# Performance work log

Measured on AMD Instinct MI355X. Metric: run time of the kernel, lower is better.

## Reference

```python
import math
import jax, jax.numpy as jnp
import numpy as np

B, S, D, H = 128, 512, 768, 12
DH = D // H  # 64


def setup_inputs() -> dict:
    key = jax.random.key(0)
    k1, k2, k3, k4, k5 = jax.random.split(key, 5)
    return {
        "X": jax.random.normal(k1, (B, S, D), jnp.float32),
        "W_qkv": jax.random.normal(k2, (3 * D, D), jnp.float32) * 0.02,
        "b_qkv": jax.random.normal(k3, (3 * D,), jnp.float32) * 0.02,
        "W_dense": jax.random.normal(k4, (D, D), jnp.float32) * 0.02,
        "b_dense": jax.random.normal(k5, (D,), jnp.float32) * 0.02,
    }


def reference(X, W_qkv, b_qkv, W_dense, b_dense):
    # Faithful translation of SelfAttention.forward (including its unusual
    # seq/batch layout: scores are [S*H, B, B] and the tril mask FILLS the
    # lower triangle with -10000, exactly as masked_fill_(tril, -1e4) does).
    b, s, d = X.shape
    qkv = jnp.einsum('bsd,ed->bse', X, W_qkv) + b_qkv            # [B,S,3D]
    qkv = qkv.reshape(b, s, H, 3 * DH)
    q = qkv[..., :DH]
    k = qkv[..., DH:2 * DH]
    v = qkv[..., 2 * DH:]
    q = q.reshape(b, s * H, DH).transpose(1, 0, 2)               # [S*H,B,DH]
    k = k.reshape(b, s * H, DH).transpose(1, 0, 2)
    v = v.reshape(b, s * H, DH).transpose(1, 0, 2)
    scores = jnp.einsum('nbd,ncd->nbc', q, k) / math.sqrt(DH)    # [S*H,B,B]
    scores = scores.reshape(s, H, b, b)
    tril = jnp.tril(jnp.ones((s, b, b), bool))[:, None]          # [S,1,B,B]
    scores = jnp.where(tril, jnp.float32(-10000.0), scores)
    probs = jax.nn.softmax(scores, axis=-1).reshape(s * H, b, b)
    ctx = jnp.einsum('nbc,ncd->nbd', probs, v)                   # [S*H,B,DH]
    ctx = ctx.reshape(s, H, b, DH).transpose(2, 0, 1, 3).reshape(b, s, d)
    out = jnp.einsum('bsd,ed->bse', ctx, W_dense)                # bias NOT added
    return (out, b_dense)
```

## Files before the change

kernel.cpp:

```cpp
#include <hip/hip_runtime.h>
#include <hip/hip_bf16.h>
#include <cstdint>
#include <cstddef>


typedef __attribute__((ext_vector_type(8))) short bf16x8_t;
typedef __attribute__((ext_vector_type(4))) float f32x4_t;

__device__ inline unsigned short f2bf(float x) {
  union { float f; unsigned int u; } v; v.f = x;
  return (unsigned short)((v.u + 0x7FFFu + ((v.u >> 16) & 1u)) >> 16);
}

#define GLL16(gp, lp) __builtin_amdgcn_global_load_lds(                      \
    (const __attribute__((address_space(1))) void*)(gp),                     \
    (__attribute__((address_space(3))) void*)(lp), 16, 0, 0)

__device__ __forceinline__ void bar() {
  asm volatile("" ::: "memory");
  __builtin_amdgcn_s_barrier();
  asm volatile("" ::: "memory");
}
#define WAITV(n) asm volatile("s_waitcnt vmcnt(" #n ")" ::: "memory")

__global__ __launch_bounds__(256) void cvt_kernel(const float* __restrict__ in,
                                                  unsigned short* __restrict__ out,
                                                  int n4) {
  int i = blockIdx.x * 256 + threadIdx.x;
  if (i >= n4) return;
  const float4 v = ((const float4*)in)[i];
  ushort4 o;
  o.x = f2bf(v.x); o.y = f2bf(v.y); o.z = f2bf(v.z); o.w = f2bf(v.w);
  ((ushort4*)out)[i] = o;
}

__global__ void bias_tail(const float* __restrict__ b, float* __restrict__ out) {
  int i = blockIdx.x * 256 + threadIdx.x;
  if (i < 768) out[(size_t)128 * 512 * 768 + i] = b[i];
}

template <bool BF16OUT>
__global__ __launch_bounds__(512, 2) void gemm256(
    const unsigned short* __restrict__ A,
    const unsigned short* __restrict__ Bt,
    const float* __restrict__ bias,
    unsigned short* __restrict__ outB,
    float* __restrict__ outF,
    const int ldo) {
  __shared__ unsigned short As[2 * 16384];
  __shared__ unsigned short Bs[2 * 16384];

  const int tid = threadIdx.x;
  const int wave = tid >> 6, lane = tid & 63;
  const int lane15 = lane & 15, quad = lane >> 4;
  const int wm = wave >> 2, wn = wave & 3;
  const int mBase = blockIdx.y * 256;
  const int nBase = blockIdx.x * 256;

  f32x4_t acc[8][4];
#pragma unroll
  for (int i = 0; i < 8; ++i)
#pragma unroll
    for (int j = 0; j < 4; ++j) { f32x4_t z = {0.f, 0.f, 0.f, 0.f}; acc[i][j] = z; }

  const unsigned short* Ag = A + (size_t)(mBase + wave * 32 + lane15) * 768 + quad * 8;
  const unsigned short* Bg = Bt + (size_t)(nBase + wave * 32 + lane15) * 768 + quad * 8;

#define STAGE_A(t_, ro_) do {                                                 \
    const unsigned short* s_ = Ag + (size_t)(ro_) * (16 * 768) + (t_) * 64;   \
    unsigned short* d_ = &As[(((t_) & 1) << 14) + (2 * wave + (ro_)) * 1024]; \
    GLL16(s_, d_); GLL16(s_ + 32, d_ + 512);                                  \
  } while (0)
#define STAGE_B(t_, ro_) do {                                                 \
    const unsigned short* s_ = Bg + (size_t)(ro_) * (16 * 768) + (t_) * 64;   \
    unsigned short* d_ = &Bs[(((t_) & 1) << 14) + (2 * wave + (ro_)) * 1024]; \
    GLL16(s_, d_); GLL16(s_ + 32, d_ + 512);                                  \
  } while (0)

  const unsigned short* aB = &As[(wm * 8) * 1024 + lane * 8];
  const unsigned short* bB = &Bs[(wn * 4) * 1024 + lane * 8];
#define RA(buf_, im_, kk_) (*(const bf16x8_t*)&aB[(buf_) + ((im_) * 2 + (kk_)) * 512])
#define RB(buf_, in_, kk_) (*(const bf16x8_t*)&bB[(buf_) + ((in_) * 2 + (kk_)) * 512])

  STAGE_A(0, 0); STAGE_A(0, 1); STAGE_B(0, 0); STAGE_B(0, 1);
  STAGE_A(1, 0);
  WAITV(2);
  bar();

  const int NT = 12;
#pragma unroll 1
  for (int t = 0; t < NT; ++t) {
    const int buf = (t & 1) << 14;
    bf16x8_t a0[4], b0[4];
#pragma unroll
    for (int im = 0; im < 4; ++im) a0[im] = RA(buf, im, 0);
#pragma unroll
    for (int in = 0; in < 4; ++in) b0[in] = RB(buf, in, 0);
    if (t + 1 < NT) STAGE_A(t + 1, 1);
    bar();
    __builtin_amdgcn_s_setprio(1);
#pragma unroll
    for (int im = 0; im < 4; ++im)
#pragma unroll
      for (int in = 0; in < 4; ++in)
        acc[im][in] = __builtin_amdgcn_mfma_f32_16x16x32_bf16(a0[im], b0[in], acc[im][in], 0, 0, 0);
    __builtin_amdgcn_s_setprio(0);
    bar();
    bf16x8_t a1[4], a0k[4], b1[4];
#pragma unroll
    for (int im = 0; im < 4; ++im) a1[im] = RA(buf, im + 4, 0);
#pragma unroll
    for (int im = 0; im < 4; ++im) a0k[im] = RA(buf, im, 1);
#pragma unroll
    for (int in = 0; in < 4; ++in) b1[in] = RB(buf, in, 1);
    if (t + 1 < NT) STAGE_B(t + 1, 0);
    bar();
    __builtin_amdgcn_s_setprio(1);
#pragma unroll
    for (int im = 0; im < 4; ++im)
#pragma unroll
      for (int in = 0; in < 4; ++in)
        acc[im + 4][in] = __builtin_amdgcn_mfma_f32_16x16x32_bf16(a1[im], b0[in], acc[im + 4][in], 0, 0, 0);
    __builtin_amdgcn_s_setprio(0);
    bar();
    bf16x8_t a1k[4];
#pragma unroll
    for (int im = 0; im < 4; ++im) a1k[im] = RA(buf, im + 4, 1);
    if (t + 1 < NT) STAGE_B(t + 1, 1);
    bar();
    __builtin_amdgcn_s_setprio(1);
#pragma unroll
    for (int im = 0; im < 4; ++im)
#pragma unroll
      for (int in = 0; in < 4; ++in)
        acc[im][in] = __builtin_amdgcn_mfma_f32_16x16x32_bf16(a0k[im], b1[in], acc[im][in], 0, 0, 0);
    __builtin_amdgcn_s_setprio(0);
    bar();
    if (t + 2 < NT) STAGE_A(t + 2, 0);
    bar();
    __builtin_amdgcn_s_setprio(1);
#pragma unroll
    for (int im = 0; im < 4; ++im)
#pragma unroll
      for (int in = 0; in < 4; ++in)
        acc[im + 4][in] = __builtin_amdgcn_mfma_f32_16x16x32_bf16(a1k[im], b1[in], acc[im + 4][in], 0, 0, 0);
    __builtin_amdgcn_s_setprio(0);
    if (t < NT - 1) {
      if (t + 2 < NT) { WAITV(2); } else { WAITV(0); }
      bar();
    }
  }
#undef STAGE_A
#undef STAGE_B
#undef RA
#undef RB

  if constexpr (BF16OUT) {
    float bv[4];
#pragma unroll
    for (int in = 0; in < 4; ++in) bv[in] = bias[nBase + wn * 64 + in * 16 + lane15];
#pragma unroll
    for (int im = 0; im < 8; ++im) {
#pragma unroll
      for (int r = 0; r < 4; ++r) {
        const int m = mBase + wm * 128 + im * 16 + quad * 4 + r;
        unsigned short* orow = outB + (size_t)m * ldo + nBase + wn * 64 + lane15;
#pragma unroll
        for (int in = 0; in < 4; ++in)
          orow[in * 16] = f2bf(acc[im][in][r] + bv[in]);
      }
    }
  } else {
#pragma unroll
    for (int im = 0; im < 8; ++im) {
#pragma unroll
      for (int r = 0; r < 4; ++r) {
        const int m = mBase + wm * 128 + im * 16 + quad * 4 + r;
        float* orow = outF + (size_t)m * ldo + nBase + wn * 64 + lane15;
#pragma unroll
        for (int in = 0; in < 4; ++in)
          orow[in * 16] = acc[im][in][r];
      }
    }
  }
}

__global__ __launch_bounds__(256) void attn_kernel(
    const unsigned short* __restrict__ QKV,
    unsigned short* __restrict__ Ctx) {
  __shared__ unsigned short Qs[128 * 72];
  __shared__ unsigned short Ks[128 * 72];

  const int n = blockIdx.x;
  const int s = n / 12;
  const int h = n - s * 12;
  const int tid = threadIdx.x;
  const int wave = tid >> 6, lane = tid & 63;
  const int lane15 = lane & 15, quad = lane >> 4;

#pragma unroll
  for (int it = 0; it < 4; ++it) {
    const int idx = it * 256 + tid;
    const int bb = idx >> 3, seg = idx & 7;
    const size_t g = (size_t)(bb * 512 + s) * 2304 + h * 192 + seg * 8;
    *(uint4*)&Qs[bb * 72 + seg * 8] = *(const uint4*)&QKV[g];
    *(uint4*)&Ks[bb * 72 + seg * 8] = *(const uint4*)&QKV[g + 64];
  }
  __syncthreads();

  f32x4_t sc[2][8];
#pragma unroll
  for (int im = 0; im < 2; ++im)
#pragma unroll
    for (int in = 0; in < 8; ++in) { f32x4_t z = {0.f, 0.f, 0.f, 0.f}; sc[im][in] = z; }

#pragma unroll
  for (int kk = 0; kk < 2; ++kk) {
    bf16x8_t a0 = *(const bf16x8_t*)&Qs[(wave * 32 + lane15) * 72 + kk * 32 + quad * 8];
    bf16x8_t a1 = *(const bf16x8_t*)&Qs[(wave * 32 + 16 + lane15) * 72 + kk * 32 + quad * 8];
#pragma unroll
    for (int in = 0; in < 8; ++in) {
      bf16x8_t b = *(const bf16x8_t*)&Ks[(in * 16 + lane15) * 72 + kk * 32 + quad * 8];
      sc[0][in] = __builtin_amdgcn_mfma_f32_16x16x32_bf16(a0, b, sc[0][in], 0, 0, 0);
      sc[1][in] = __builtin_amdgcn_mfma_f32_16x16x32_bf16(a1, b, sc[1][in], 0, 0, 0);
    }
  }
  __syncthreads();

  unsigned short* Vt = Ks;
  unsigned short* Ps = Qs;
  {
    const int c = tid & 127, half = tid >> 7;
    const size_t vb = (size_t)(c * 512 + s) * 2304 + h * 192 + 128;
#pragma unroll
    for (int dd = 0; dd < 4; ++dd) {
      const int dseg = half * 4 + dd;
      uint4 v = *(const uint4*)&QKV[vb + dseg * 8];
      const unsigned short* pv = (const unsigned short*)&v;
#pragma unroll
      for (int j = 0; j < 8; ++j) Vt[(dseg * 8 + j) * 136 + c] = pv[j];
    }
  }

  unsigned short* myP = Ps + wave * 16 * 136;

#pragma unroll 1
  for (int im = 0; im < 2; ++im) {
#pragma unroll
    for (int r = 0; r < 4; ++r) {
      const int row = wave * 32 + im * 16 + quad * 4 + r;
      float vals[8];
      float mx = -3.0e38f;
#pragma unroll
      for (int in = 0; in < 8; ++in) {
        const int col = in * 16 + lane15;
        float v = sc[im][in][r] * 0.125f;
        v = (col <= row) ? -10000.0f : v;
        vals[in] = v;
        mx = fmaxf(mx, v);
      }
      mx = fmaxf(mx, __shfl_xor(mx, 1, 16));
      mx = fmaxf(mx, __shfl_xor(mx, 2, 16));
      mx = fmaxf(mx, __shfl_xor(mx, 4, 16));
      mx = fmaxf(mx, __shfl_xor(mx, 8, 16));
      float sum = 0.f;
#pragma unroll
      for (int in = 0; in < 8; ++in) {
        const float e_ = __expf(vals[in] - mx);
        vals[in] = e_;
        sum += e_;
      }
      sum += __shfl_xor(sum, 1, 16);
      sum += __shfl_xor(sum, 2, 16);
      sum += __shfl_xor(sum, 4, 16);
      sum += __shfl_xor(sum, 8, 16);
      const float inv = 1.0f / sum;
#pragma unroll
      for (int in = 0; in < 8; ++in)
        myP[(quad * 4 + r) * 136 + in * 16 + lane15] = f2bf(vals[in] * inv);
    }
    __syncthreads();

    f32x4_t oc[4];
#pragma unroll
    for (int nt = 0; nt < 4; ++nt) { f32x4_t z = {0.f, 0.f, 0.f, 0.f}; oc[nt] = z; }
#pragma unroll
    for (int kk = 0; kk < 4; ++kk) {
      bf16x8_t a = *(const bf16x8_t*)&myP[lane15 * 136 + kk * 32 + quad * 8];
#pragma unroll
      for (int nt = 0; nt < 4; ++nt) {
        bf16x8_t b = *(const bf16x8_t*)&Vt[(nt * 16 + lane15) * 136 + kk * 32 + quad * 8];
        oc[nt] = __builtin_amdgcn_mfma_f32_16x16x32_bf16(a, b, oc[nt], 0, 0, 0);
      }
    }
#pragma unroll
    for (int nt = 0; nt < 4; ++nt) {
#pragma unroll
      for (int r = 0; r < 4; ++r) {
        const int bb = wave * 32 + im * 16 + quad * 4 + r;
        Ctx[((size_t)bb * 512 + s) * 768 + h * 64 + nt * 16 + lane15] = f2bf(oc[nt][r]);
      }
    }
    __syncthreads();
  }
}

extern "C" void kernel_launch(void* const* d_in, const int* in_sizes, int n_in,
                              void* d_out, int out_size, void* d_ws, size_t ws_size,
                              hipStream_t stream) {
  const float* X    = (const float*)d_in[0];
  const float* Wqkv = (const float*)d_in[1];
  const float* bqkv = (const float*)d_in[2];
  const float* Wd   = (const float*)d_in[3];
  const float* bd   = (const float*)d_in[4];
  float* out = (float*)d_out;

  char* ws = (char*)d_ws;
  unsigned short* Xb  = (unsigned short*)(ws);
  unsigned short* QKV = (unsigned short*)(ws + 100663296);
  unsigned short* Wqb = (unsigned short*)(ws + 402653184);
  unsigned short* Wdb = (unsigned short*)(ws + 406192128);

  cvt_kernel<<<dim3(49152), 256, 0, stream>>>(X, Xb, 12582912);
  cvt_kernel<<<dim3(1728), 256, 0, stream>>>(Wqkv, Wqb, 442368);
  cvt_kernel<<<dim3(576), 256, 0, stream>>>(Wd, Wdb, 147456);
  bias_tail<<<dim3(3), 256, 0, stream>>>(bd, out);

  gemm256<true><<<dim3(9, 256), 512, 0, stream>>>(Xb, Wqb, bqkv, QKV, nullptr, 2304);
  attn_kernel<<<dim3(6144), 256, 0, stream>>>(QKV, Xb );
  gemm256<false><<<dim3(3, 256), 512, 0, stream>>>(Xb, Wdb, nullptr, nullptr, out, 768);
}
```

Before: 1.101 ms.

## Remap GEMM workgroups across XCDs and issue whole next K-tile prefetch upfront

```diff
diff --git a/kernel.cpp b/kernel.cpp
--- a/kernel.cpp
+++ b/kernel.cpp
@@ -46,7 +46,7 @@
     const float* __restrict__ bias,
     unsigned short* __restrict__ outB,
     float* __restrict__ outF,
-    const int ldo) {
+    const int ldo, const int nbn) {
   __shared__ unsigned short As[2 * 16384];
   __shared__ unsigned short Bs[2 * 16384];
 
@@ -54,8 +54,14 @@
   const int wave = tid >> 6, lane = tid & 63;
   const int lane15 = lane & 15, quad = lane >> 4;
   const int wm = wave >> 2, wn = wave & 3;
-  const int mBase = blockIdx.y * 256;
-  const int nBase = blockIdx.x * 256;
+
+  const int wg = blockIdx.y * nbn + blockIdx.x;
+  const int chunk = (nbn << 8) >> 3;
+  const int w = (wg & 7) * chunk + (wg >> 3);
+  const int mTile = w / nbn;
+  const int nTile = w - mTile * nbn;
+  const int mBase = mTile * 256;
+  const int nBase = nTile * 256;
 
   f32x4_t acc[8][4];
 #pragma unroll
@@ -66,15 +72,16 @@
   const unsigned short* Ag = A + (size_t)(mBase + wave * 32 + lane15) * 768 + quad * 8;
   const unsigned short* Bg = Bt + (size_t)(nBase + wave * 32 + lane15) * 768 + quad * 8;
 
-#define STAGE_A(t_, ro_) do {                                                 \
-    const unsigned short* s_ = Ag + (size_t)(ro_) * (16 * 768) + (t_) * 64;   \
-    unsigned short* d_ = &As[(((t_) & 1) << 14) + (2 * wave + (ro_)) * 1024]; \
-    GLL16(s_, d_); GLL16(s_ + 32, d_ + 512);                                  \
-  } while (0)
-#define STAGE_B(t_, ro_) do {                                                 \
-    const unsigned short* s_ = Bg + (size_t)(ro_) * (16 * 768) + (t_) * 64;   \
-    unsigned short* d_ = &Bs[(((t_) & 1) << 14) + (2 * wave + (ro_)) * 1024]; \
-    GLL16(s_, d_); GLL16(s_ + 32, d_ + 512);                                  \
+#define STAGE_T(t_) do {                                                       \
+    const int bo_ = ((t_) & 1) << 14;                                          \
+    const unsigned short* sa_ = Ag + (t_) * 64;                                \
+    unsigned short* da_ = &As[bo_ + 2 * wave * 1024];                          \
+    GLL16(sa_, da_);                    GLL16(sa_ + 32, da_ + 512);            \
+    GLL16(sa_ + 16 * 768, da_ + 1024);  GLL16(sa_ + 16 * 768 + 32, da_ + 1536);\
+    const unsigned short* sb_ = Bg + (t_) * 64;                                \
+    unsigned short* db_ = &Bs[bo_ + 2 * wave * 1024];                          \
+    GLL16(sb_, db_);                    GLL16(sb_ + 32, db_ + 512);            \
+    GLL16(sb_ + 16 * 768, db_ + 1024);  GLL16(sb_ + 16 * 768 + 32, db_ + 1536);\
   } while (0)
 
   const unsigned short* aB = &As[(wm * 8) * 1024 + lane * 8];
@@ -82,21 +89,20 @@
 #define RA(buf_, im_, kk_) (*(const bf16x8_t*)&aB[(buf_) + ((im_) * 2 + (kk_)) * 512])
 #define RB(buf_, in_, kk_) (*(const bf16x8_t*)&bB[(buf_) + ((in_) * 2 + (kk_)) * 512])
 
-  STAGE_A(0, 0); STAGE_A(0, 1); STAGE_B(0, 0); STAGE_B(0, 1);
-  STAGE_A(1, 0);
-  WAITV(2);
+  STAGE_T(0);
+  WAITV(0);
   bar();
 
   const int NT = 12;
 #pragma unroll 1
   for (int t = 0; t < NT; ++t) {
     const int buf = (t & 1) << 14;
+    if (t + 1 < NT) STAGE_T(t + 1);
     bf16x8_t a0[4], b0[4];
 #pragma unroll
     for (int im = 0; im < 4; ++im) a0[im] = RA(buf, im, 0);
 #pragma unroll
     for (int in = 0; in < 4; ++in) b0[in] = RB(buf, in, 0);
-    if (t + 1 < NT) STAGE_A(t + 1, 1);
     bar();
     __builtin_amdgcn_s_setprio(1);
 #pragma unroll
@@ -106,14 +112,11 @@
         acc[im][in] = __builtin_amdgcn_mfma_f32_16x16x32_bf16(a0[im], b0[in], acc[im][in], 0, 0, 0);
     __builtin_amdgcn_s_setprio(0);
     bar();
-    bf16x8_t a1[4], a0k[4], b1[4];
+    bf16x8_t a1[4], a0k[4];
 #pragma unroll
     for (int im = 0; im < 4; ++im) a1[im] = RA(buf, im + 4, 0);
 #pragma unroll
     for (int im = 0; im < 4; ++im) a0k[im] = RA(buf, im, 1);
-#pragma unroll
-    for (int in = 0; in < 4; ++in) b1[in] = RB(buf, in, 1);
-    if (t + 1 < NT) STAGE_B(t + 1, 0);
     bar();
     __builtin_amdgcn_s_setprio(1);
 #pragma unroll
@@ -123,10 +126,11 @@
         acc[im + 4][in] = __builtin_amdgcn_mfma_f32_16x16x32_bf16(a1[im], b0[in], acc[im + 4][in], 0, 0, 0);
     __builtin_amdgcn_s_setprio(0);
     bar();
-    bf16x8_t a1k[4];
+    bf16x8_t b1[4], a1k[4];
+#pragma unroll
+    for (int in = 0; in < 4; ++in) b1[in] = RB(buf, in, 1);
 #pragma unroll
     for (int im = 0; im < 4; ++im) a1k[im] = RA(buf, im + 4, 1);
-    if (t + 1 < NT) STAGE_B(t + 1, 1);
     bar();
     __builtin_amdgcn_s_setprio(1);
 #pragma unroll
@@ -136,8 +140,6 @@
         acc[im][in] = __builtin_amdgcn_mfma_f32_16x16x32_bf16(a0k[im], b1[in], acc[im][in], 0, 0, 0);
     __builtin_amdgcn_s_setprio(0);
     bar();
-    if (t + 2 < NT) STAGE_A(t + 2, 0);
-    bar();
     __builtin_amdgcn_s_setprio(1);
 #pragma unroll
     for (int im = 0; im < 4; ++im)
@@ -145,13 +147,12 @@
       for (int in = 0; in < 4; ++in)
         acc[im + 4][in] = __builtin_amdgcn_mfma_f32_16x16x32_bf16(a1k[im], b1[in], acc[im + 4][in], 0, 0, 0);
     __builtin_amdgcn_s_setprio(0);
-    if (t < NT - 1) {
-      if (t + 2 < NT) { WAITV(2); } else { WAITV(0); }
+    if (t + 1 < NT) {
+      WAITV(0);
       bar();
     }
   }
-#undef STAGE_A
-#undef STAGE_B
+#undef STAGE_T
 #undef RA
 #undef RB
 
@@ -326,7 +327,7 @@
   cvt_kernel<<<dim3(576), 256, 0, stream>>>(Wd, Wdb, 147456);
   bias_tail<<<dim3(3), 256, 0, stream>>>(bd, out);
 
-  gemm256<true><<<dim3(9, 256), 512, 0, stream>>>(Xb, Wqb, bqkv, QKV, nullptr, 2304);
+  gemm256<true><<<dim3(9, 256), 512, 0, stream>>>(Xb, Wqb, bqkv, QKV, nullptr, 2304, 9);
   attn_kernel<<<dim3(6144), 256, 0, stream>>>(QKV, Xb );
-  gemm256<false><<<dim3(3, 256), 512, 0, stream>>>(Xb, Wdb, nullptr, nullptr, out, 768);
-}
+  gemm256<false><<<dim3(3, 256), 512, 0, stream>>>(Xb, Wdb, nullptr, nullptr, out, 768, 3);
+}
```

Result: slower. 1.225 ms (+11.2%).
